# Optimization experiments

Measured on AMD Instinct MI355X. Metric: run time of the kernel, lower is better.

The kernel has to match this reference:

```python
import jax, jax.numpy as jnp
import numpy as np


def setup_inputs() -> dict:
    key = jax.random.key(0)
    # Uniform in (0.9, 1.1) so the running product over 8192 elements stays finite.
    x = jax.random.uniform(key, (4096, 8192), dtype=jnp.float32, minval=0.9, maxval=1.1)
    return {"x": x}


def reference(x) -> jnp.ndarray:
    # Inclusive prefix product along dim 1 (matches cumprod_dim1_cuda / torch.cumprod(x, dim=1)).
    return jnp.cumprod(x, axis=1)
```

## Files before the change

kernel.cpp:

```cpp
#include <hip/hip_runtime.h>


#define N      8192
#define T      512
#define NW     (T / 64)
#define QV     (N / (T * 4))

typedef float f32x4 __attribute__((ext_vector_type(4)));

__global__ __launch_bounds__(T) void cumprod_rows_kernel(
    const float* __restrict__ x, float* __restrict__ out, int n_rows)
{
    __shared__ float wsum[NW];

    const int row = blockIdx.x;
    if (row >= n_rows) return;
    const int tid  = threadIdx.x;
    const int lane = tid & 63;
    const int wid  = tid >> 6;

    const float* __restrict__ xr   = x   + (size_t)row * N + (size_t)wid * (N / NW);
    float*       __restrict__ outr = out + (size_t)row * N + (size_t)wid * (N / NW);

    f32x4 d[QV];
#pragma unroll
    for (int v = 0; v < QV; ++v)
        d[v] = *reinterpret_cast<const f32x4*>(xr + (v * 64 + lane) * 4);

    float carry = 1.0f;
    float coef[QV];
#pragma unroll
    for (int v = 0; v < QV; ++v) {
        d[v].y *= d[v].x;
        d[v].z *= d[v].y;
        d[v].w *= d[v].z;
        float inc = d[v].w;
#pragma unroll
        for (int off = 1; off < 64; off <<= 1) {
            const float o = __shfl_up(inc, off, 64);
            if (lane >= off) inc *= o;
        }
        float ex = __shfl_up(inc, 1, 64);
        if (lane == 0) ex = 1.0f;
        coef[v] = carry * ex;
        carry  *= __shfl(inc, 63, 64);
    }

    if (lane == 63) wsum[wid] = carry;
    __syncthreads();

    float wpre = 1.0f;
#pragma unroll
    for (int w = 0; w < NW - 1; ++w)
        if (w < wid) wpre *= wsum[w];

#pragma unroll
    for (int v = 0; v < QV; ++v) {
        const float f = wpre * coef[v];
        f32x4 o = d[v];
        o.x *= f; o.y *= f; o.z *= f; o.w *= f;
        __builtin_nontemporal_store(o, reinterpret_cast<f32x4*>(outr + (v * 64 + lane) * 4));
    }
}

extern "C" void kernel_launch(void* const* d_in, const int* in_sizes, int n_in,
                              void* d_out, int out_size, void* d_ws, size_t ws_size,
                              hipStream_t stream)
{
    const float* x   = (const float*)d_in[0];
    float*       out = (float*)d_out;
    const int n_rows = in_sizes[0] / N;
    cumprod_rows_kernel<<<n_rows, T, 0, stream>>>(x, out, n_rows);
}
```

Before: 231.6 us.

## Process four rows per block with register prefetch of next row

Each block now handles four consecutive rows and loads the next row into registers while it scans and stores the current one, with the shared warp-sum buffer double-buffered. The aim is to overlap global load latency with compute and cut block launch overhead. In exchange the grid is four times smaller (1024 blocks), which may hurt occupancy and latency hiding, and register pressure doubles. The row-bounds check is dropped, so it assumes the row count is divisible by four.

```diff
diff --git a/kernel.cpp b/kernel.cpp
--- a/kernel.cpp
+++ b/kernel.cpp
@@ -1,65 +1,83 @@
 #include <hip/hip_runtime.h>
 
 
-#define N      8192
-#define T      512
-#define NW     (T / 64)
-#define QV     (N / (T * 4))
+#define N    8192
+#define T    512
+#define NW   (T / 64)
+#define QV   (N / (T * 4))
+#define RPB  4
 
 typedef float f32x4 __attribute__((ext_vector_type(4)));
 
 __global__ __launch_bounds__(T) void cumprod_rows_kernel(
     const float* __restrict__ x, float* __restrict__ out, int n_rows)
 {
-    __shared__ float wsum[NW];
+    __shared__ float wsum[2][NW];
 
-    const int row = blockIdx.x;
-    if (row >= n_rows) return;
     const int tid  = threadIdx.x;
     const int lane = tid & 63;
     const int wid  = tid >> 6;
 
-    const float* __restrict__ xr   = x   + (size_t)row * N + (size_t)wid * (N / NW);
-    float*       __restrict__ outr = out + (size_t)row * N + (size_t)wid * (N / NW);
+    const size_t base = (size_t)blockIdx.x * RPB * N + (size_t)wid * (N / NW);
+    const float* __restrict__ xr   = x   + base;
+    float*       __restrict__ outr = out + base;
 
-    f32x4 d[QV];
+    f32x4 A[QV];
 #pragma unroll
     for (int v = 0; v < QV; ++v)
-        d[v] = *reinterpret_cast<const f32x4*>(xr + (v * 64 + lane) * 4);
-
-    float carry = 1.0f;
-    float coef[QV];
-#pragma unroll
-    for (int v = 0; v < QV; ++v) {
-        d[v].y *= d[v].x;
-        d[v].z *= d[v].y;
-        d[v].w *= d[v].z;
-        float inc = d[v].w;
-#pragma unroll
-        for (int off = 1; off < 64; off <<= 1) {
-            const float o = __shfl_up(inc, off, 64);
-            if (lane >= off) inc *= o;
-        }
-        float ex = __shfl_up(inc, 1, 64);
-        if (lane == 0) ex = 1.0f;
-        coef[v] = carry * ex;
-        carry  *= __shfl(inc, 63, 64);
-    }
-
-    if (lane == 63) wsum[wid] = carry;
-    __syncthreads();
-
-    float wpre = 1.0f;
-#pragma unroll
-    for (int w = 0; w < NW - 1; ++w)
-        if (w < wid) wpre *= wsum[w];
+        A[v] = *reinterpret_cast<const f32x4*>(xr + (v * 64 + lane) * 4);
 
 #pragma unroll
-    for (int v = 0; v < QV; ++v) {
-        const float f = wpre * coef[v];
-        f32x4 o = d[v];
-        o.x *= f; o.y *= f; o.z *= f; o.w *= f;
-        __builtin_nontemporal_store(o, reinterpret_cast<f32x4*>(outr + (v * 64 + lane) * 4));
+    for (int r = 0; r < RPB; ++r) {
+        f32x4 B[QV];
+        if (r + 1 < RPB) {
+            const float* __restrict__ xn = xr + (size_t)(r + 1) * N;
+#pragma unroll
+            for (int v = 0; v < QV; ++v)
+                B[v] = *reinterpret_cast<const f32x4*>(xn + (v * 64 + lane) * 4);
+        }
+
+        float carry = 1.0f;
+        float coef[QV];
+#pragma unroll
+        for (int v = 0; v < QV; ++v) {
+            A[v].y *= A[v].x;
+            A[v].z *= A[v].y;
+            A[v].w *= A[v].z;
+            float inc = A[v].w;
+#pragma unroll
+            for (int off = 1; off < 64; off <<= 1) {
+                const float o = __shfl_up(inc, off, 64);
+                if (lane >= off) inc *= o;
+            }
+            float ex = __shfl_up(inc, 1, 64);
+            if (lane == 0) ex = 1.0f;
+            coef[v] = carry * ex;
+            carry  *= __shfl(inc, 63, 64);
+        }
+
+        if (lane == 63) wsum[r & 1][wid] = carry;
+        __syncthreads();
+
+        float wpre = 1.0f;
+#pragma unroll
+        for (int w = 0; w < NW - 1; ++w)
+            if (w < wid) wpre *= wsum[r & 1][w];
+
+        float* __restrict__ outrr = outr + (size_t)r * N;
+#pragma unroll
+        for (int v = 0; v < QV; ++v) {
+            const float f = wpre * coef[v];
+            f32x4 o = A[v];
+            o.x *= f; o.y *= f; o.z *= f; o.w *= f;
+            __builtin_nontemporal_store(
+                o, reinterpret_cast<f32x4*>(outrr + (v * 64 + lane) * 4));
+        }
+
+        if (r + 1 < RPB) {
+#pragma unroll
+            for (int v = 0; v < QV; ++v) A[v] = B[v];
+        }
     }
 }
 
@@ -70,5 +88,5 @@
     const float* x   = (const float*)d_in[0];
     float*       out = (float*)d_out;
     const int n_rows = in_sizes[0] / N;
-    cumprod_rows_kernel<<<n_rows, T, 0, stream>>>(x, out, n_rows);
+    cumprod_rows_kernel<<<n_rows / RPB, T, 0, stream>>>(x, out, n_rows);
 }
```

New measurement: 235.8 us. About the same (+1.8%).

## Use DPP-based wave scan and halve block size to 256 threads

Applied to the files above, without the earlier changes.

Replaces the shuffle-based (ds_bpermute) intra-wave multiplicative scan with a DPP row-shift/row-broadcast scan using identity 1.0 for out-of-range lanes. It builds an exclusive scan by shifting each lane's chunk total first, and gets the wave total via readlane. The block size drops from 512 to 256 threads, so each wave handles twice as many float4 vectors, raising per-thread register use and work. The aim is to cut the latency of the cross-lane scan and the LDS traffic, at the cost of lower thread-level parallelism per row.

```diff
diff --git a/kernel.cpp b/kernel.cpp
--- a/kernel.cpp
+++ b/kernel.cpp
@@ -1,12 +1,36 @@
 #include <hip/hip_runtime.h>
 
 
-#define N      8192
-#define T      512
-#define NW     (T / 64)
-#define QV     (N / (T * 4))
+#define N    8192
+#define T    256
+#define NW   (T / 64)
+#define SEG  (N / NW)
+#define QV   (SEG / 256)
 
 typedef float f32x4 __attribute__((ext_vector_type(4)));
+
+__device__ __forceinline__ float readlane63(float x) {
+    return __builtin_bit_cast(float,
+        __builtin_amdgcn_readlane(__builtin_bit_cast(int, x), 63));
+}
+
+template<int CTRL, int RM, int BM>
+__device__ __forceinline__ float dpp_id1(float x) {
+    int r = __builtin_amdgcn_update_dpp(
+        __builtin_bit_cast(int, 1.0f), __builtin_bit_cast(int, x),
+        CTRL, RM, BM, false);
+    return __builtin_bit_cast(float, r);
+}
+
+__device__ __forceinline__ float wave_scan_mul(float x) {
+    x *= dpp_id1<0x111, 0xf, 0xf>(x);
+    x *= dpp_id1<0x112, 0xf, 0xf>(x);
+    x *= dpp_id1<0x114, 0xf, 0xf>(x);
+    x *= dpp_id1<0x118, 0xf, 0xf>(x);
+    x *= dpp_id1<0x142, 0xa, 0xf>(x);
+    x *= dpp_id1<0x143, 0xc, 0xf>(x);
+    return x;
+}
 
 __global__ __launch_bounds__(T) void cumprod_rows_kernel(
     const float* __restrict__ x, float* __restrict__ out, int n_rows)
@@ -19,34 +43,41 @@
     const int lane = tid & 63;
     const int wid  = tid >> 6;
 
-    const float* __restrict__ xr   = x   + (size_t)row * N + (size_t)wid * (N / NW);
-    float*       __restrict__ outr = out + (size_t)row * N + (size_t)wid * (N / NW);
+    const size_t base = (size_t)row * N + (size_t)wid * SEG;
+    const float* __restrict__ xr   = x   + base;
+    float*       __restrict__ outr = out + base;
 
     f32x4 d[QV];
 #pragma unroll
     for (int v = 0; v < QV; ++v)
-        d[v] = *reinterpret_cast<const f32x4*>(xr + (v * 64 + lane) * 4);
+        d[v] = *reinterpret_cast<const f32x4*>(xr + v * 256 + lane * 4);
+
+    float t[QV];
+#pragma unroll
+    for (int v = 0; v < QV; ++v) {
+        d[v].y *= d[v].x;
+        d[v].z *= d[v].y;
+        d[v].w *= d[v].z;
+        t[v] = d[v].w;
+    }
+
+    float ep[QV];
+#pragma unroll
+    for (int v = 0; v < QV; ++v) {
+        const float e = __shfl_up(t[v], 1, 64);
+        ep[v] = (lane == 0) ? 1.0f : e;
+    }
 
     float carry = 1.0f;
     float coef[QV];
 #pragma unroll
     for (int v = 0; v < QV; ++v) {
-        d[v].y *= d[v].x;
-        d[v].z *= d[v].y;
-        d[v].w *= d[v].z;
-        float inc = d[v].w;
-#pragma unroll
-        for (int off = 1; off < 64; off <<= 1) {
-            const float o = __shfl_up(inc, off, 64);
-            if (lane >= off) inc *= o;
-        }
-        float ex = __shfl_up(inc, 1, 64);
-        if (lane == 0) ex = 1.0f;
-        coef[v] = carry * ex;
-        carry  *= __shfl(inc, 63, 64);
+        const float exc = wave_scan_mul(ep[v]);
+        coef[v] = carry * exc;
+        carry  *= readlane63(exc * t[v]);
     }
 
-    if (lane == 63) wsum[wid] = carry;
+    if (lane == 0) wsum[wid] = carry;
     __syncthreads();
 
     float wpre = 1.0f;
@@ -59,7 +90,8 @@
         const float f = wpre * coef[v];
         f32x4 o = d[v];
         o.x *= f; o.y *= f; o.z *= f; o.w *= f;
-        __builtin_nontemporal_store(o, reinterpret_cast<f32x4*>(outr + (v * 64 + lane) * 4));
+        __builtin_nontemporal_store(
+            o, reinterpret_cast<f32x4*>(outr + v * 256 + lane * 4));
     }
 }
 
```

After: 232.7 us. Within noise of the previous version (+0.5%).
